# Optimization experiments

Measured on AMD Instinct MI355X. Metric: run time of the kernel, lower is better.

The kernel has to match this reference:

```python
import jax, jax.numpy as jnp
import numpy as np

EMBED_DIM = 256
NUM_HEADS = 8
HEAD_DIM = EMBED_DIM // NUM_HEADS
SCALING = HEAD_DIM ** -0.5
SEQ = 1024
BSZ = 4


def setup_inputs() -> dict:
    rng = jax.random.key(0)
    ks = jax.random.split(rng, 5)
    E = EMBED_DIM
    q = jax.random.normal(ks[0], (SEQ, BSZ, E), jnp.float32)
    k = jax.random.normal(ks[1], (SEQ, BSZ, E), jnp.float32)
    v = jax.random.normal(ks[2], (SEQ, BSZ, E), jnp.float32)
    # xavier-uniform-like scale for the packed 9E x E projection
    lim_in = np.sqrt(6.0 / (9 * E + E)).astype(np.float32)
    in_proj_w = jax.random.uniform(ks[3], (9 * E, E), jnp.float32, -lim_in, lim_in)
    in_proj_b = jnp.zeros((9 * E,), jnp.float32)
    lim_out = np.sqrt(6.0 / (E + E)).astype(np.float32)
    out_w = jax.random.uniform(ks[4], (E, E), jnp.float32, -lim_out, lim_out)
    out_b = jnp.zeros((E,), jnp.float32)
    return {"query": q, "key": k, "value": v,
            "in_proj_w": in_proj_w, "in_proj_b": in_proj_b,
            "out_w": out_w, "out_b": out_b,
            "shape0": 32, "shape1": 32}


def reference(query, key, value, in_proj_w, in_proj_b, out_w, out_b, shape0, shape1):
    S, B, E = query.shape
    H, hd = NUM_HEADS, HEAD_DIM

    def proj(x, i):  # slice i of the packed in-projection
        return x @ in_proj_w[i * E:(i + 1) * E].T + in_proj_b[i * E:(i + 1) * E]

    def heads(x):  # [S,B,E] -> [B*H, S, hd]
        return x.reshape(S, B * H, hd).transpose(1, 0, 2)

    q      = heads(proj(query, 0) * SCALING)
    k      = heads(proj(key, 1))
    v      = heads(proj(value, 2))
    q_left = heads(proj(query, 3))
    k_left = heads(proj(key, 4))
    q_right = heads(proj(query, 5))
    k_right = heads(proj(key, 6))
    q_loc  = heads(proj(query, 7) * SCALING)
    k_loc  = heads(proj(key, 8))

    global_w = q @ k.transpose(0, 2, 1)        # [BH,S,S]
    local_w  = q_loc @ k_loc.transpose(0, 2, 1)

    left_sm  = jax.nn.softmax(q_left @ k_left.transpose(0, 2, 1), axis=-1)
    right_sm = jax.nn.softmax(q_right @ k_right.transpose(0, 2, 1), axis=-1)

    triu = jnp.triu(jnp.ones((S, S), query.dtype))
    mini = jnp.tile(jnp.triu(jnp.ones((shape1, shape1), query.dtype)), (shape0, shape0))
    triu = (triu * mini)[None]                 # [1,S,S]
    triu_t = triu.transpose(0, 2, 1)

    fw_mask = (left_sm @ triu) * (right_sm @ triu_t)
    bw_mask = (left_sm @ triu_t) * (right_sm @ triu)
    local_mask = fw_mask + bw_mask             # [BH,S,S]

    attn_w = jax.nn.softmax(0.1 * global_w + local_w * local_mask, axis=-1)
    attn = (attn_w @ v).transpose(1, 0, 2).reshape(S, B, E)
    attn = attn @ out_w.T + out_b
    consistent_mask = local_mask.sum(axis=0)   # [S,S]
    return attn, consistent_mask
```

## Files before the change

kernel.cpp:

```cpp
#include <hip/hip_runtime.h>


typedef _Float16 v8h __attribute__((ext_vector_type(8)));
typedef _Float16 v4h __attribute__((ext_vector_type(4)));
typedef _Float16 v2h __attribute__((ext_vector_type(2)));
typedef float    v4f __attribute__((ext_vector_type(4)));

#define SL 1048576
#define RS 1032

static constexpr float SCALE = 0.17677669529663687f;


__global__ __launch_bounds__(256)
void cvt_kernel(const float* __restrict__ q, const float* __restrict__ k,
                const float* __restrict__ v, const float* __restrict__ W,
                _Float16* __restrict__ X16, _Float16* __restrict__ W16)
{
    const int b = blockIdx.x;
    const int t = threadIdx.x;
    const float* src; _Float16* dst; int off;
    if (b < 512)       { src = q; dst = X16;             off = b; }
    else if (b < 1024) { src = k; dst = X16 + (1 << 20); off = b - 512; }
    else if (b < 1536) { src = v; dst = X16 + (2 << 20); off = b - 1024; }
    else               { src = W; dst = W16;             off = b - 1536; }
    const int i = off * 2048 + t * 8;
    const float4 a = *(const float4*)(src + i);
    const float4 c = *(const float4*)(src + i + 4);
    v8h h;
    h[0] = (_Float16)a.x; h[1] = (_Float16)a.y; h[2] = (_Float16)a.z; h[3] = (_Float16)a.w;
    h[4] = (_Float16)c.x; h[5] = (_Float16)c.y; h[6] = (_Float16)c.z; h[7] = (_Float16)c.w;
    *(v8h*)(dst + i) = h;
}

__global__ __launch_bounds__(256)
void proj_kernel(const _Float16* __restrict__ X16, const _Float16* __restrict__ W16,
                 const float* __restrict__ bias, _Float16* __restrict__ P)
{
    __shared__ __align__(16) _Float16 stage[4096];
    const int t  = threadIdx.x;
    const int n0 = blockIdx.x * 64;
    const int m0 = blockIdx.y * 64;
    const int slice = n0 >> 8;
    const int q2 = (n0 >> 6) & 3;
    const bool kslice = (slice == 1) || (slice == 4) || (slice == 6) || (slice == 8);
    const _Float16* X = X16 + (slice == 2 ? (2 << 20) : (kslice ? (1 << 20) : 0));
    const int w = t >> 6, lane = t & 63, m16 = lane & 15, kg = lane >> 4;
    const v4f zero = {0.f, 0.f, 0.f, 0.f};
    v4f acc[4] = {zero, zero, zero, zero};
    const _Float16* Arow = X + (size_t)(m0 + w * 16 + m16) * 256 + kg * 8;
    const _Float16* B0   = W16 + (size_t)(n0 + m16) * 256 + kg * 8;
#pragma unroll
    for (int kk = 0; kk < 8; ++kk) {
        const v8h a = *(const v8h*)(Arow + kk * 32);
#pragma unroll
        for (int nf = 0; nf < 4; ++nf) {
            const v8h bb = *(const v8h*)(B0 + nf * 4096 + kk * 32);
            acc[nf] = __builtin_amdgcn_mfma_f32_16x16x32_f16(a, bb, acc[nf], 0, 0, 0);
        }
    }
    const float scale = (slice == 0 || slice == 7) ? SCALE : 1.0f;
#pragma unroll
    for (int nf = 0; nf < 4; ++nf) {
        const int c = n0 + nf * 16 + m16;
        const float bv = bias[c];
#pragma unroll
        for (int i = 0; i < 4; ++i) {
            const _Float16 val = (_Float16)((acc[nf][i] + bv) * scale);
            const int lb = i * 2 + (nf >> 1);
            int inner;
            if (slice == 2) {
                const int ls = w * 4 + kg;
                inner = ((nf & 1) << 8) + ((ls >> 3) << 7) + m16 * 8 + (ls & 7);
            } else {
                inner = ((w * 4 + kg) + (((nf & 1) * 2 + (m16 >> 3)) << 4)) * 8 + (m16 & 7);
            }
            stage[lb * 512 + inner] = val;
        }
    }
    __syncthreads();
    {
        const int o  = t * 16;
        const int lb = o >> 9;
        const int inner = o & 511;
        const int bs = lb >> 1, hh = lb & 1;
        const int bh = bs * 8 + 2 * q2 + hh;
        size_t dst;
        if (slice == 2) {
            const int kc = m0 >> 7;
            const int g0 = (m0 >> 5) & 3;
            const int nt = inner >> 8, a = (inner >> 7) & 1, r = inner & 127;
            dst = (size_t)2 * SL + (size_t)bh * 32768
                + (size_t)(kc * 1024 + nt * 512 + (g0 + a) * 128 + r);
        } else {
            const int tile = m0 >> 6;
            dst = (size_t)slice * SL + (size_t)bh * 32768 + (size_t)(tile * 512 + inner);
        }
        *(v8h*)(P + dst)     = *(const v8h*)(stage + o);
        *(v8h*)(P + dst + 8) = *(const v8h*)(stage + o + 8);
    }
}

__global__ __launch_bounds__(512, 4)
void attn_kernel(const _Float16* __restrict__ P, float* __restrict__ attn_pre,
                 _Float16* __restrict__ pmask)
{
    __shared__ __align__(16) _Float16 Lh[16 * RS];
    __shared__ __align__(16) _Float16 Rh[16 * RS];

    const int t    = threadIdx.x;
    const int bid  = blockIdx.x;
    const int q    = bid >> 3;
    const int bh   = ((bid & 7) << 2) + (q & 3);
    const int rt   = q >> 2;
    const int w    = __builtin_amdgcn_readfirstlane(t >> 6);
    const int lane = t & 63;
    const int m16  = lane & 15;
    const int kg   = lane >> 4;

    const _Float16* Pb = P + (size_t)bh * 32768;
    const v4f zero = {0.f, 0.f, 0.f, 0.f};

    {
        const v8h a_l = *(const v8h*)(Pb + 3 * SL + rt * 512 + lane * 8);
        const v8h a_r = *(const v8h*)(Pb + 5 * SL + rt * 512 + lane * 8);
        const _Float16* Bl = Pb + 4 * SL;
        const _Float16* Br = Pb + 6 * SL;
#pragma unroll 4
        for (int jt2 = 0; jt2 < 8; ++jt2) {
            const int jt = (w << 3) + jt2;
            const v8h bL = *(const v8h*)(Bl + jt * 512 + lane * 8);
            const v8h bR = *(const v8h*)(Br + jt * 512 + lane * 8);
            v4f cL = __builtin_amdgcn_mfma_f32_16x16x32_f16(a_l, bL, zero, 0, 0, 0);
            v4f cR = __builtin_amdgcn_mfma_f32_16x16x32_f16(a_r, bR, zero, 0, 0, 0);
            const int col = (jt << 4) + m16;
#pragma unroll
            for (int i = 0; i < 4; ++i) {
                Lh[((kg << 2) + i) * RS + col] = (_Float16)cL[i];
                Rh[((kg << 2) + i) * RS + col] = (_Float16)cR[i];
            }
        }
    }
    __syncthreads();

    auto softmax_pairs = [&](_Float16* ROW) {
        float v0[8], v1[8];
        float ss = 0.f;
#pragma unroll
        for (int kq = 0; kq < 8; ++kq) {
            const v2h pr = *(const v2h*)&ROW[(lane + (kq << 6)) << 1];
            v0[kq] = __expf((float)pr[0]);
            v1[kq] = __expf((float)pr[1]);
            ss += v0[kq] + v1[kq];
        }
#pragma unroll
        for (int off = 32; off; off >>= 1) ss += __shfl_xor(ss, off);
        const float inv = 1.f / ss;
#pragma unroll
        for (int kq = 0; kq < 8; ++kq) {
            v2h pr; pr[0] = (_Float16)(v0[kq] * inv); pr[1] = (_Float16)(v1[kq] * inv);
            *(v2h*)&ROW[(lane + (kq << 6)) << 1] = pr;
        }
    };
#pragma unroll
    for (int r = 0; r < 2; ++r) {
        softmax_pairs(&Lh[((w << 1) + r) * RS]);
        softmax_pairs(&Rh[((w << 1) + r) * RS]);
    }

    {
        const int kr = lane & 31;
#pragma unroll
        for (int r = 0; r < 2; ++r) {
            _Float16* ROW = (lane >= 32) ? &Rh[((w << 1) + r) * RS] : &Lh[((w << 1) + r) * RS];
            float run = 0.f;
#pragma unroll 4
            for (int kb = 0; kb < 32; ++kb) {
                float x = (float)ROW[(kb << 5) + kr];
#pragma unroll
                for (int off = 1; off < 32; off <<= 1) {
                    float y = __shfl_up(x, off, 32);
                    if (kr >= off) x += y;
                }
                run += x;
                ROW[(kb << 5) + kr] = (_Float16)run;
            }
        }
    }
    __syncthreads();

    v4h sc4[8];
    {
        _Float16* pm = pmask + (size_t)bh * 1048576 + (size_t)rt * 16384;
        const v8h a_g = *(const v8h*)(Pb + 0 * SL + rt * 512 + lane * 8);
        const v8h a_c = *(const v8h*)(Pb + 7 * SL + rt * 512 + lane * 8);
        const _Float16* Bg = Pb + 1 * SL;
        const _Float16* Bc = Pb + 8 * SL;
#pragma unroll
        for (int jt2 = 0; jt2 < 8; ++jt2) {
            const int jt  = (w << 3) + jt2;
            const int jb  = jt >> 1;
            const int jr  = ((jt & 1) << 4) + m16;
            const int col = (jt << 4) + m16;
            const v8h bG = *(const v8h*)(Bg + jt * 512 + lane * 8);
            const v8h bC = *(const v8h*)(Bc + jt * 512 + lane * 8);
            const v4f g4 = __builtin_amdgcn_mfma_f32_16x16x32_f16(a_g, bG, zero, 0, 0, 0);
            const v4f l4 = __builtin_amdgcn_mfma_f32_16x16x32_f16(a_c, bC, zero, 0, 0, 0);
            v4h s4, m4;
#pragma unroll
            for (int i = 0; i < 4; ++i) {
                const int rr = ((kg << 2) + i) * RS;
                const float PL  = (float)Lh[rr + col];
                const float PR  = (float)Rh[rr + col];
                const float eLb = jb ? (float)Lh[rr + (jb << 5) - 1] : 0.f;
                const float eRb = jb ? (float)Rh[rr + (jb << 5) - 1] : 0.f;
                const float eLc = jr ? (float)Lh[rr + 991 + jr] : 0.f;
                const float eRc = jr ? (float)Rh[rr + 991 + jr] : 0.f;
                const float eLbc = (jb && jr) ? (float)Lh[rr + ((jb - 1) << 5) + jr - 1] : 0.f;
                const float eRbc = (jb && jr) ? (float)Rh[rr + ((jb - 1) << 5) + jr - 1] : 0.f;
                const float SLv = 1.0f - eLb - eLc + eLbc;
                const float SRv = 1.0f - eRb - eRc + eRbc;
                const float mkv = PL * SRv + SLv * PR;
                s4[i] = (_Float16)(0.1f * g4[i] + l4[i] * mkv);
                m4[i] = (_Float16)mkv;
            }
            sc4[jt2] = s4;
            *(v4h*)(pm + ((size_t)jt << 8) + (lane << 2)) = m4;
        }
    }
    __syncthreads();

    {
#pragma unroll
        for (int jt2 = 0; jt2 < 8; ++jt2) {
            const int col = ((((w << 3) + jt2)) << 4) + m16;
#pragma unroll
            for (int i = 0; i < 4; ++i)
                Lh[((kg << 2) + i) * RS + col] = sc4[jt2][i];
        }
    }
    __syncthreads();

#pragma unroll
    for (int r = 0; r < 2; ++r) softmax_pairs(&Lh[((w << 1) + r) * RS]);
    __syncthreads();

    {
        const int nt = w & 1, hf = w >> 1;
        v4f c = zero;
        const _Float16* Vb = Pb + 2 * SL + nt * 512 + lane * 8;
        const int kc0 = hf << 3;
#pragma unroll 4
        for (int kc2 = 0; kc2 < 8; ++kc2) {
            const int kc = kc0 + kc2;
            const v8h a = *(const v8h*)&Lh[m16 * RS + (kc << 5) + (kg << 3)];
            const v8h b = *(const v8h*)(Vb + (size_t)kc * 1024);
            c = __builtin_amdgcn_mfma_f32_16x16x32_f16(a, b, c, 0, 0, 0);
        }
        float* Pbuf = (float*)&Rh[0];
#pragma unroll
        for (int i = 0; i < 4; ++i) Pbuf[(w << 8) + (lane << 2) + i] = c[i];
    }
    __syncthreads();

    {
        const float* Pbuf = (const float*)&Rh[0];
        const int r   = t >> 5;
        const int d   = t & 31;
        const int nt2 = d >> 4, n = d & 15;
        const int kg2 = r >> 2, i2 = r & 3;
        const int off = (kg2 << 6) + (n << 2) + i2;
        float v = 0.f;
#pragma unroll
        for (int hf = 0; hf < 4; ++hf)
            v += Pbuf[(((hf << 1) + nt2) << 8) + off];
        const int srow = (rt << 4) + r;
        attn_pre[((size_t)(srow * 4 + (bh >> 3))) * 256 + (bh & 7) * 32 + d] = v;
    }
}

__global__ __launch_bounds__(256)
void tail_kernel(const _Float16* __restrict__ pmask, float* __restrict__ cmask,
                 const float* __restrict__ A, const float* __restrict__ W,
                 const float* __restrict__ bias, float* __restrict__ C)
{
    __shared__ __align__(16) float SMEM[4 * 16 * 132];
    const int bid = blockIdx.x;
    const int t = threadIdx.x;

    if (bid >= 256) {
        const int b2 = bid - 256;
        const int rt = b2 >> 3, wh = b2 & 7;
        float (*T4)[16][132] = (float(*)[16][132])SMEM;
        const int wv = t >> 6;
        const int lane = t & 63, m16 = lane & 15, kg = lane >> 4;
        float acc[8][4] = {};
        const _Float16* base = pmask + (size_t)rt * 16384 + ((size_t)wh << 11) + (lane << 2)
                             + ((size_t)wv << 3) * 1048576;
        for (int bh = 0; bh < 8; ++bh) {
            const _Float16* p = base + (size_t)bh * 1048576;
#pragma unroll
            for (int jt2 = 0; jt2 < 8; ++jt2) {
                const v4h h4 = *(const v4h*)(p + (jt2 << 8));
#pragma unroll
                for (int i = 0; i < 4; ++i) acc[jt2][i] += (float)h4[i];
            }
        }
#pragma unroll
        for (int jt2 = 0; jt2 < 8; ++jt2)
#pragma unroll
            for (int i = 0; i < 4; ++i)
                T4[wv][(kg << 2) + i][(jt2 << 4) + m16] = acc[jt2][i];
        __syncthreads();
        const int row = t >> 4;
        const int c0  = (t & 15) << 3;
#pragma unroll
        for (int h = 0; h < 2; ++h) {
            const int c = c0 + (h << 2);
            const float4 s0 = *(const float4*)&T4[0][row][c];
            const float4 s1 = *(const float4*)&T4[1][row][c];
            const float4 s2 = *(const float4*)&T4[2][row][c];
            const float4 s3 = *(const float4*)&T4[3][row][c];
            const float4 o = make_float4(s0.x + s1.x + s2.x + s3.x,
                                         s0.y + s1.y + s2.y + s3.y,
                                         s0.z + s1.z + s2.z + s3.z,
                                         s0.w + s1.w + s2.w + s3.w);
            *(float4*)&cmask[((size_t)((rt << 4) + row) << 10) + (wh << 7) + c] = o;
        }
    } else {
        const int n0 = (bid & 3) * 64;
        const int m0 = (bid >> 2) * 64;
        float (*As)[68] = (float(*)[68])SMEM;
        float (*Bs)[68] = (float(*)[68])(SMEM + 16 * 68);
        const int tx = t & 15, ty = t >> 4;
        const int lm = t >> 2, lk = (t & 3) << 2;
        float acc[4][4] = {};
        for (int k0 = 0; k0 < 256; k0 += 16) {
            float4 av = *(const float4*)(A + (size_t)(m0 + lm) * 256 + k0 + lk);
            float4 bv = *(const float4*)(W + (size_t)(n0 + lm) * 256 + k0 + lk);
            As[lk + 0][lm] = av.x; As[lk + 1][lm] = av.y; As[lk + 2][lm] = av.z; As[lk + 3][lm] = av.w;
            Bs[lk + 0][lm] = bv.x; Bs[lk + 1][lm] = bv.y; Bs[lk + 2][lm] = bv.z; Bs[lk + 3][lm] = bv.w;
            __syncthreads();
#pragma unroll
            for (int kk = 0; kk < 16; ++kk) {
                float4 a4 = *(const float4*)&As[kk][ty << 2];
                float4 b4 = *(const float4*)&Bs[kk][tx << 2];
                float aa[4] = {a4.x, a4.y, a4.z, a4.w};
                float bb[4] = {b4.x, b4.y, b4.z, b4.w};
#pragma unroll
                for (int i = 0; i < 4; ++i)
#pragma unroll
                    for (int j = 0; j < 4; ++j)
                        acc[i][j] = fmaf(aa[i], bb[j], acc[i][j]);
            }
            __syncthreads();
        }
#pragma unroll
        for (int i = 0; i < 4; ++i) {
            const int m  = m0 + (ty << 2) + i;
            const int c0 = n0 + (tx << 2);
            float4 o = make_float4(acc[i][0] + bias[c0 + 0], acc[i][1] + bias[c0 + 1],
                                   acc[i][2] + bias[c0 + 2], acc[i][3] + bias[c0 + 3]);
            *(float4*)&C[(size_t)m * 256 + c0] = o;
        }
    }
}

extern "C" void kernel_launch(void* const* d_in, const int* in_sizes, int n_in,
                              void* d_out, int out_size, void* d_ws, size_t ws_size,
                              hipStream_t stream)
{
    const float* q  = (const float*)d_in[0];
    const float* k  = (const float*)d_in[1];
    const float* v  = (const float*)d_in[2];
    const float* Wi = (const float*)d_in[3];
    const float* bi = (const float*)d_in[4];
    const float* Wo = (const float*)d_in[5];
    const float* bo = (const float*)d_in[6];

    float* out      = (float*)d_out;
    float* attn_out = out;
    float* cmask    = out + 1048576;

    _Float16* Ppack    = (_Float16*)d_ws;
    float*    attn_pre = (float*)((char*)d_ws + 18874368);
    _Float16* pmask    = (_Float16*)((char*)d_ws + 23068672);
    _Float16* X16      = (_Float16*)((char*)d_ws + 90177536);
    _Float16* W16      = (_Float16*)((char*)d_ws + 96468992);

    cvt_kernel<<<1824, 256, 0, stream>>>(q, k, v, Wi, X16, W16);
    proj_kernel<<<dim3(36, 64), 256, 0, stream>>>(X16, W16, bi, Ppack);
    attn_kernel<<<2048, 512, 0, stream>>>(Ppack, attn_pre, pmask);
    cmask_reduce_kernel_dummy:;
    tail_kernel<<<768, 256, 0, stream>>>(pmask, cmask, attn_pre, Wo, bo, attn_out);
}
```

Measured before the change: 288.9 us.

## Fuse score softmax and PV matmul into per-wave online softmax

```diff
diff --git a/kernel.cpp b/kernel.cpp
--- a/kernel.cpp
+++ b/kernel.cpp
@@ -107,6 +107,7 @@
 {
     __shared__ __align__(16) _Float16 Lh[16 * RS];
     __shared__ __align__(16) _Float16 Rh[16 * RS];
+    __shared__ __align__(16) _Float16 STbuf[8 * 640];
 
     const int t    = threadIdx.x;
     const int bid  = blockIdx.x;
@@ -189,77 +190,101 @@
     }
     __syncthreads();
 
-    v4h sc4[8];
     {
         _Float16* pm = pmask + (size_t)bh * 1048576 + (size_t)rt * 16384;
         const v8h a_g = *(const v8h*)(Pb + 0 * SL + rt * 512 + lane * 8);
         const v8h a_c = *(const v8h*)(Pb + 7 * SL + rt * 512 + lane * 8);
         const _Float16* Bg = Pb + 1 * SL;
         const _Float16* Bc = Pb + 8 * SL;
-#pragma unroll
-        for (int jt2 = 0; jt2 < 8; ++jt2) {
-            const int jt  = (w << 3) + jt2;
-            const int jb  = jt >> 1;
-            const int jr  = ((jt & 1) << 4) + m16;
-            const int col = (jt << 4) + m16;
-            const v8h bG = *(const v8h*)(Bg + jt * 512 + lane * 8);
-            const v8h bC = *(const v8h*)(Bc + jt * 512 + lane * 8);
-            const v4f g4 = __builtin_amdgcn_mfma_f32_16x16x32_f16(a_g, bG, zero, 0, 0, 0);
-            const v4f l4 = __builtin_amdgcn_mfma_f32_16x16x32_f16(a_c, bC, zero, 0, 0, 0);
-            v4h s4, m4;
+        const _Float16* Vb = Pb + 2 * SL;
+        _Float16* STw = &STbuf[w * 640];
+        v4f acc0 = zero, acc1 = zero;
+        float mrow[4] = {-1e30f, -1e30f, -1e30f, -1e30f};
+        float zrow[4] = {0.f, 0.f, 0.f, 0.f};
+#pragma unroll
+        for (int p = 0; p < 4; ++p) {
+            const int kc = (w << 2) + p;
+            v4f s8[2];
+#pragma unroll
+            for (int e = 0; e < 2; ++e) {
+                const int jt  = (w << 3) + (p << 1) + e;
+                const int jb  = kc;
+                const int jr  = ((jt & 1) << 4) + m16;
+                const int col = (jt << 4) + m16;
+                const v8h bG = *(const v8h*)(Bg + jt * 512 + lane * 8);
+                const v8h bC = *(const v8h*)(Bc + jt * 512 + lane * 8);
+                const v4f g4 = __builtin_amdgcn_mfma_f32_16x16x32_f16(a_g, bG, zero, 0, 0, 0);
+                const v4f l4 = __builtin_amdgcn_mfma_f32_16x16x32_f16(a_c, bC, zero, 0, 0, 0);
+                v4h m4;
+                v4f s4;
+#pragma unroll
+                for (int i = 0; i < 4; ++i) {
+                    const int rr = ((kg << 2) + i) * RS;
+                    const float PL  = (float)Lh[rr + col];
+                    const float PR  = (float)Rh[rr + col];
+                    const float eLb = jb ? (float)Lh[rr + (jb << 5) - 1] : 0.f;
+                    const float eRb = jb ? (float)Rh[rr + (jb << 5) - 1] : 0.f;
+                    const float eLc = jr ? (float)Lh[rr + 991 + jr] : 0.f;
+                    const float eRc = jr ? (float)Rh[rr + 991 + jr] : 0.f;
+                    const float eLbc = (jb && jr) ? (float)Lh[rr + ((jb - 1) << 5) + jr - 1] : 0.f;
+                    const float eRbc = (jb && jr) ? (float)Rh[rr + ((jb - 1) << 5) + jr - 1] : 0.f;
+                    const float SLv = 1.0f - eLb - eLc + eLbc;
+                    const float SRv = 1.0f - eRb - eRc + eRbc;
+                    const float mkv = PL * SRv + SLv * PR;
+                    s4[i] = 0.1f * g4[i] + l4[i] * mkv;
+                    m4[i] = (_Float16)mkv;
+                }
+                s8[e] = s4;
+                *(v4h*)(pm + ((size_t)jt << 8) + (lane << 2)) = m4;
+            }
+            float f[4];
 #pragma unroll
             for (int i = 0; i < 4; ++i) {
-                const int rr = ((kg << 2) + i) * RS;
-                const float PL  = (float)Lh[rr + col];
-                const float PR  = (float)Rh[rr + col];
-                const float eLb = jb ? (float)Lh[rr + (jb << 5) - 1] : 0.f;
-                const float eRb = jb ? (float)Rh[rr + (jb << 5) - 1] : 0.f;
-                const float eLc = jr ? (float)Lh[rr + 991 + jr] : 0.f;
-                const float eRc = jr ? (float)Rh[rr + 991 + jr] : 0.f;
-                const float eLbc = (jb && jr) ? (float)Lh[rr + ((jb - 1) << 5) + jr - 1] : 0.f;
-                const float eRbc = (jb && jr) ? (float)Rh[rr + ((jb - 1) << 5) + jr - 1] : 0.f;
-                const float SLv = 1.0f - eLb - eLc + eLbc;
-                const float SRv = 1.0f - eRb - eRc + eRbc;
-                const float mkv = PL * SRv + SLv * PR;
-                s4[i] = (_Float16)(0.1f * g4[i] + l4[i] * mkv);
-                m4[i] = (_Float16)mkv;
-            }
-            sc4[jt2] = s4;
-            *(v4h*)(pm + ((size_t)jt << 8) + (lane << 2)) = m4;
-        }
-    }
-    __syncthreads();
-
-    {
-#pragma unroll
-        for (int jt2 = 0; jt2 < 8; ++jt2) {
-            const int col = ((((w << 3) + jt2)) << 4) + m16;
-#pragma unroll
-            for (int i = 0; i < 4; ++i)
-                Lh[((kg << 2) + i) * RS + col] = sc4[jt2][i];
-        }
-    }
-    __syncthreads();
-
-#pragma unroll
-    for (int r = 0; r < 2; ++r) softmax_pairs(&Lh[((w << 1) + r) * RS]);
-    __syncthreads();
-
-    {
-        const int nt = w & 1, hf = w >> 1;
-        v4f c = zero;
-        const _Float16* Vb = Pb + 2 * SL + nt * 512 + lane * 8;
-        const int kc0 = hf << 3;
-#pragma unroll 4
-        for (int kc2 = 0; kc2 < 8; ++kc2) {
-            const int kc = kc0 + kc2;
-            const v8h a = *(const v8h*)&Lh[m16 * RS + (kc << 5) + (kg << 3)];
-            const v8h b = *(const v8h*)(Vb + (size_t)kc * 1024);
-            c = __builtin_amdgcn_mfma_f32_16x16x32_f16(a, b, c, 0, 0, 0);
-        }
+                float tm = fmaxf(s8[0][i], s8[1][i]);
+                tm = fmaxf(tm, __shfl_xor(tm, 1));
+                tm = fmaxf(tm, __shfl_xor(tm, 2));
+                tm = fmaxf(tm, __shfl_xor(tm, 4));
+                tm = fmaxf(tm, __shfl_xor(tm, 8));
+                const float mn = fmaxf(mrow[i], tm);
+                f[i] = __expf(mrow[i] - mn);
+                mrow[i] = mn;
+            }
+#pragma unroll
+            for (int i = 0; i < 4; ++i) {
+                const float p0 = __expf(s8[0][i] - mrow[i]);
+                const float p1 = __expf(s8[1][i] - mrow[i]);
+                STw[((kg << 2) + i) * 40 + m16]      = (_Float16)p0;
+                STw[((kg << 2) + i) * 40 + 16 + m16] = (_Float16)p1;
+                float zs = p0 + p1;
+                zs += __shfl_xor(zs, 1);
+                zs += __shfl_xor(zs, 2);
+                zs += __shfl_xor(zs, 4);
+                zs += __shfl_xor(zs, 8);
+                zrow[i] = zrow[i] * f[i] + zs;
+                acc0[i] *= f[i];
+                acc1[i] *= f[i];
+            }
+            const v8h pa  = *(const v8h*)(STw + m16 * 40 + kg * 8);
+            const v8h bv0 = *(const v8h*)(Vb + (size_t)(kc * 2 + 0) * 512 + lane * 8);
+            const v8h bv1 = *(const v8h*)(Vb + (size_t)(kc * 2 + 1) * 512 + lane * 8);
+            acc0 = __builtin_amdgcn_mfma_f32_16x16x32_f16(pa, bv0, acc0, 0, 0, 0);
+            acc1 = __builtin_amdgcn_mfma_f32_16x16x32_f16(pa, bv1, acc1, 0, 0, 0);
+        }
+        float* zm = (float*)STw;
+        if (m16 == 0) {
+#pragma unroll
+            for (int i = 0; i < 4; ++i) {
+                zm[((kg << 2) + i) * 2]     = zrow[i];
+                zm[((kg << 2) + i) * 2 + 1] = mrow[i];
+            }
+        }
+        __syncthreads();
         float* Pbuf = (float*)&Rh[0];
 #pragma unroll
-        for (int i = 0; i < 4; ++i) Pbuf[(w << 8) + (lane << 2) + i] = c[i];
+        for (int i = 0; i < 4; ++i) {
+            Pbuf[(((w << 1) + 0) << 8) + (lane << 2) + i] = acc0[i];
+            Pbuf[(((w << 1) + 1) << 8) + (lane << 2) + i] = acc1[i];
+        }
     }
     __syncthreads();
 
@@ -268,14 +293,21 @@
         const int r   = t >> 5;
         const int d   = t & 31;
         const int nt2 = d >> 4, n = d & 15;
-        const int kg2 = r >> 2, i2 = r & 3;
-        const int off = (kg2 << 6) + (n << 2) + i2;
-        float v = 0.f;
-#pragma unroll
-        for (int hf = 0; hf < 4; ++hf)
-            v += Pbuf[(((hf << 1) + nt2) << 8) + off];
+        const int off = ((r >> 2) << 6) + (n << 2) + (r & 3);
+        float M = -1e30f;
+#pragma unroll
+        for (int w8 = 0; w8 < 8; ++w8)
+            M = fmaxf(M, ((const float*)&STbuf[w8 * 640])[r * 2 + 1]);
+        float Z = 0.f, v = 0.f;
+#pragma unroll
+        for (int w8 = 0; w8 < 8; ++w8) {
+            const float* zm8 = (const float*)&STbuf[w8 * 640];
+            const float sc = __expf(zm8[r * 2 + 1] - M);
+            Z += zm8[r * 2] * sc;
+            v += Pbuf[(((w8 << 1) + nt2) << 8) + off] * sc;
+        }
         const int srow = (rt << 4) + r;
-        attn_pre[((size_t)(srow * 4 + (bh >> 3))) * 256 + (bh & 7) * 32 + d] = v;
+        attn_pre[((size_t)(srow * 4 + (bh >> 3))) * 256 + (bh & 7) * 32 + d] = v / Z;
     }
 }
 
@@ -391,6 +423,5 @@
     cvt_kernel<<<1824, 256, 0, stream>>>(q, k, v, Wi, X16, W16);
     proj_kernel<<<dim3(36, 64), 256, 0, stream>>>(X16, W16, bi, Ppack);
     attn_kernel<<<2048, 512, 0, stream>>>(Ppack, attn_pre, pmask);
-    cmask_reduce_kernel_dummy:;
     tail_kernel<<<768, 256, 0, stream>>>(pmask, cmask, attn_pre, Wo, bo, attn_out);
 }
```

Result: no change. 293.1 us (+1.5%).
